# Performance work log

Measured on AMD Instinct MI355X. Metric: run time of the kernel, lower is better.

The kernel has to match this reference:

```python
import jax, jax.numpy as jnp
import numpy as np

K = 3
STRIDE = 1
PAD = 1


def _unfold(x, k, stride, pad):
    # x: (B, C, H, W) -> (B, C*k*k, L) matching torch.nn.functional.unfold
    # ordering: channel slowest, then kh, then kw.
    B, C, H, W = x.shape
    Hout = (H + 2 * pad - k) // stride + 1
    Wout = (W + 2 * pad - k) // stride + 1
    xp = jnp.pad(x, ((0, 0), (0, 0), (pad, pad), (pad, pad)))
    patches = []  # fixed k*k loop (9 iters), not a data-dim loop
    for i in range(k):
        for j in range(k):
            patches.append(xp[:, :, i:i + stride * Hout:stride, j:j + stride * Wout:stride])
    # (B, C, k*k, Hout, Wout) -> (B, C*k*k, L)
    p = jnp.stack(patches, axis=2)
    return p.reshape(B, C * k * k, Hout * Wout), Hout, Wout


def setup_inputs() -> dict:
    key = jax.random.key(0)
    k1, k2 = jax.random.split(key)
    x = jax.random.normal(k1, (4, 32, 56, 56), dtype=jnp.float32)
    weights = jax.random.normal(k2, (64, 32, 3, 3), dtype=jnp.float32)
    return {"x": x, "weights": weights}


def reference(x, weights):
    B = x.shape[0]
    O = weights.shape[0]
    mu_w = jnp.mean(jnp.abs(weights))
    x_unf, Hout, Wout = _unfold(x, K, STRIDE, PAD)      # (B, Ckk, L)
    w_unf = weights.reshape(O, -1)                        # (O, Ckk)
    # min-plus 'convolution': broadcast min then reduce over patch dim
    min_val = jnp.minimum(x_unf[:, None, :, :], w_unf[None, :, :, None])  # (B, O, Ckk, L)
    z = mu_w * jnp.sum(min_val, axis=2)                   # (B, O, L)
    return z.reshape(B, O, Hout, Wout)
```

## Files before the change

kernel.cpp:

```cpp
#include <hip/hip_runtime.h>

#define CIN  32
#define OCH  64
#define HH   56
#define WW   56
#define BB   4
#define OT   4
#define IMG  (HH * WW)
#define NW   18432
#define PH   58
#define PW   58
#define PIMG (PH * PW)
#define NXPK (BB * (CIN/2) * PIMG)
#define XPKBLKS (NXPK / 256)
#define NWPK (OCH * (CIN/2) * 9)
#define WPKBLKS (NWPK / 256)
#define WOFFu 64
#define XOFFu (WOFFu + NWPK)

typedef _Float16 h2 __attribute__((ext_vector_type(2)));

static __device__ __forceinline__ h2 pkmin_vs(h2 xv, unsigned wu) {
    unsigned xu = __builtin_bit_cast(unsigned, xv);
    unsigned ru;
    asm("v_pk_min_f16 %0, %1, %2" : "=v"(ru) : "v"(xu), "s"(wu));
    return __builtin_bit_cast(h2, ru);
}

__global__ __launch_bounds__(256) void prep(const float* __restrict__ x,
                                            const float* __restrict__ w,
                                            float* __restrict__ ws) {
    unsigned* wsu = reinterpret_cast<unsigned*>(ws);
    if (blockIdx.x < XPKBLKS) {
        int idx = blockIdx.x * 256 + threadIdx.x;
        int bc  = idx / PIMG;
        int r   = idx - bc * PIMG;
        int ph  = r / PW;
        int pw  = r - ph * PW;
        int hh  = ph - 1, wc = pw - 1;
        float v0 = 0.f, v1 = 0.f;
        if ((unsigned)hh < (unsigned)HH && (unsigned)wc < (unsigned)WW) {
            int base = ((bc >> 4) * CIN + (bc & 15) * 2) * IMG + hh * WW + wc;
            v0 = x[base];
            v1 = x[base + IMG];
        }
        h2 p; p.x = (_Float16)v0; p.y = (_Float16)v1;
        wsu[XOFFu + idx] = __builtin_bit_cast(unsigned, p);
        return;
    }
    if (blockIdx.x < XPKBLKS + WPKBLKS) {
        int idx = (blockIdx.x - XPKBLKS) * 256 + threadIdx.x;
        int t    = idx % 9;
        int rest = idx / 9;
        int cp   = rest & 15;
        int oo   = rest >> 4;
        int base = oo * (CIN * 9) + cp * 18 + t;
        h2 p; p.x = (_Float16)w[base]; p.y = (_Float16)w[base + 9];
        wsu[WOFFu + idx] = __builtin_bit_cast(unsigned, p);
        return;
    }
    float s = 0.f;
    const float4* w4 = reinterpret_cast<const float4*>(w);
    #pragma unroll
    for (int k = 0; k < 18; ++k) {
        float4 v = w4[k * 256 + threadIdx.x];
        s += fabsf(v.x) + fabsf(v.y) + fabsf(v.z) + fabsf(v.w);
    }
    #pragma unroll
    for (int off = 32; off; off >>= 1) s += __shfl_down(s, off);
    __shared__ float sm[4];
    if ((threadIdx.x & 63) == 0) sm[threadIdx.x >> 6] = s;
    __syncthreads();
    if (threadIdx.x == 0)
        ws[0] = (sm[0] + sm[1] + sm[2] + sm[3]) * (1.0f / (float)NW);
}

__global__ __launch_bounds__(128) void minconv_kernel(const float* __restrict__ ws,
                                                      const float* __restrict__ wts,
                                                      float* __restrict__ out) {
    const unsigned* wsu = reinterpret_cast<const unsigned*>(ws);
    const int lane = threadIdx.x & 63;
    const int wv   = threadIdx.x >> 6;
    const int wvs  = __builtin_amdgcn_readfirstlane(wv);
    const int hw = blockIdx.x * 64 + lane;
    const int o0 = blockIdx.y * OT;
    const int b  = blockIdx.z;
    const int h  = hw / WW;
    const int w  = hw - h * WW;

    const float mu = ws[0];

    const int cp0 = wvs * 8;
    const unsigned* xq = wsu + XOFFu + (size_t)(b * 16 + cp0) * PIMG + h * PW + w;
    const unsigned* wq0 = wsu + WOFFu + o0 * 144 + cp0 * 9;

    h2 xall[72];
    #pragma unroll
    for (int cp = 0; cp < 8; ++cp)
        #pragma unroll
        for (int kh = 0; kh < 3; ++kh)
            #pragma unroll
            for (int kw = 0; kw < 3; ++kw)
                xall[cp * 9 + kh * 3 + kw] =
                    __builtin_bit_cast(h2, xq[cp * PIMG + kh * PW + kw]);

    h2 ones; ones.x = (_Float16)1.f; ones.y = (_Float16)1.f;
    float acc0 = 0.f, acc1 = 0.f, acc2 = 0.f, acc3 = 0.f;

    unsigned wA[36], wB[36];
    #pragma unroll
    for (int i = 0; i < 36; ++i) wA[i] = wq0[i];

    #pragma unroll
    for (int oo = 0; oo < OT; ++oo) {
        #pragma unroll
        for (int i = 0; i < 36; ++i) wB[i] = wq0[oo * 144 + 36 + i];

        float ae = 0.f, ao = 0.f;
        #pragma unroll
        for (int cp = 0; cp < 4; ++cp)
            #pragma unroll
            for (int t = 0; t < 9; ++t) {
                h2 m = pkmin_vs(xall[cp * 9 + t], wA[cp * 9 + t]);
                if (t & 1) ao = __builtin_amdgcn_fdot2(m, ones, ao, false);
                else       ae = __builtin_amdgcn_fdot2(m, ones, ae, false);
            }

        if (oo < OT - 1) {
            #pragma unroll
            for (int i = 0; i < 36; ++i) wA[i] = wq0[(oo + 1) * 144 + i];
        }

        #pragma unroll
        for (int cp = 0; cp < 4; ++cp)
            #pragma unroll
            for (int t = 0; t < 9; ++t) {
                h2 m = pkmin_vs(xall[(cp + 4) * 9 + t], wB[cp * 9 + t]);
                if (t & 1) ao = __builtin_amdgcn_fdot2(m, ones, ao, false);
                else       ae = __builtin_amdgcn_fdot2(m, ones, ae, false);
            }

        float a = ae + ao;
        switch (oo) {
            case 0: acc0 = a; break;
            case 1: acc1 = a; break;
            case 2: acc2 = a; break;
            case 3: acc3 = a; break;
        }
    }

    __shared__ float red[2][2][64];
    if (wv == 0) {
        red[0][0][lane] = acc2;
        red[0][1][lane] = acc3;
    } else {
        red[1][0][lane] = acc0;
        red[1][1][lane] = acc1;
    }
    __syncthreads();

    float* ob = out + ((size_t)b * OCH + o0) * IMG + hw;
    if (wv == 0) {
        ob[0]       = mu * (acc0 + red[1][0][lane]);
        ob[IMG]     = mu * (acc1 + red[1][1][lane]);
    } else {
        ob[2 * IMG] = mu * (acc2 + red[0][0][lane]);
        ob[3 * IMG] = mu * (acc3 + red[0][1][lane]);
    }
}

extern "C" void kernel_launch(void* const* d_in, const int* in_sizes, int n_in,
                              void* d_out, int out_size, void* d_ws, size_t ws_size,
                              hipStream_t stream) {
    const float* x   = (const float*)d_in[0];
    const float* w   = (const float*)d_in[1];
    float*       out = (float*)d_out;
    float*       ws  = (float*)d_ws;

    prep<<<XPKBLKS + WPKBLKS + 1, 256, 0, stream>>>(x, w, ws);
    dim3 grid(IMG / 64, OCH / OT, BB);
    minconv_kernel<<<grid, 128, 0, stream>>>(ws, w, out);
}
```

Measured before the change: 68.60 us.

## Sum min-products with packed fp16 adds and re-layout weights contiguously per wave

The per-element fdot2 accumulations are replaced by a tree of v_pk_add_f16 over each channel pair's nine taps. A single fdot2 then folds each partial sum into the fp32 accumulator. This cuts the reduction instruction count and shortens the dependency chain. The weight packing is reordered so each wave's weights for an output tile are contiguous, which should make the scalar weight loads simpler. The cost is that nine-term sums are now accumulated in fp16, which reduces precision.

```diff
diff --git a/kernel.cpp b/kernel.cpp
--- a/kernel.cpp
+++ b/kernel.cpp
@@ -26,6 +26,13 @@
     asm("v_pk_min_f16 %0, %1, %2" : "=v"(ru) : "v"(xu), "s"(wu));
     return __builtin_bit_cast(h2, ru);
 }
+static __device__ __forceinline__ h2 pkadd(h2 a, h2 b) {
+    unsigned au = __builtin_bit_cast(unsigned, a);
+    unsigned bu = __builtin_bit_cast(unsigned, b);
+    unsigned ru;
+    asm("v_pk_add_f16 %0, %1, %2" : "=v"(ru) : "v"(au), "v"(bu));
+    return __builtin_bit_cast(h2, ru);
+}
 
 __global__ __launch_bounds__(256) void prep(const float* __restrict__ x,
                                             const float* __restrict__ w,
@@ -50,12 +57,18 @@
     }
     if (blockIdx.x < XPKBLKS + WPKBLKS) {
         int idx = (blockIdx.x - XPKBLKS) * 256 + threadIdx.x;
-        int t    = idx % 9;
-        int rest = idx / 9;
-        int cp   = rest & 15;
-        int oo   = rest >> 4;
-        int base = oo * (CIN * 9) + cp * 18 + t;
-        h2 p; p.x = (_Float16)w[base]; p.y = (_Float16)w[base + 9];
+        int otile = idx / 576;
+        int r     = idx - otile * 576;
+        int wvq   = r / 288;
+        int r2    = r - wvq * 288;
+        int oo    = r2 / 72;
+        int r3    = r2 - oo * 72;
+        int cl    = r3 / 9;
+        int t     = r3 - cl * 9;
+        int o     = otile * OT + oo;
+        int cp    = wvq * 8 + cl;
+        int src   = o * (CIN * 9) + cp * 18 + t;
+        h2 p; p.x = (_Float16)w[src]; p.y = (_Float16)w[src + 9];
         wsu[WOFFu + idx] = __builtin_bit_cast(unsigned, p);
         return;
     }
@@ -92,7 +105,7 @@
 
     const int cp0 = wvs * 8;
     const unsigned* xq = wsu + XOFFu + (size_t)(b * 16 + cp0) * PIMG + h * PW + w;
-    const unsigned* wq0 = wsu + WOFFu + o0 * 144 + cp0 * 9;
+    const unsigned* wq0 = wsu + WOFFu + blockIdx.y * 576 + wvs * 288;
 
     h2 xall[72];
     #pragma unroll
@@ -114,33 +127,40 @@
     #pragma unroll
     for (int oo = 0; oo < OT; ++oo) {
         #pragma unroll
-        for (int i = 0; i < 36; ++i) wB[i] = wq0[oo * 144 + 36 + i];
-
-        float ae = 0.f, ao = 0.f;
-        #pragma unroll
-        for (int cp = 0; cp < 4; ++cp)
-            #pragma unroll
-            for (int t = 0; t < 9; ++t) {
-                h2 m = pkmin_vs(xall[cp * 9 + t], wA[cp * 9 + t]);
-                if (t & 1) ao = __builtin_amdgcn_fdot2(m, ones, ao, false);
-                else       ae = __builtin_amdgcn_fdot2(m, ones, ae, false);
-            }
+        for (int i = 0; i < 36; ++i) wB[i] = wq0[oo * 72 + 36 + i];
+
+        float a = 0.f;
+        #pragma unroll
+        for (int cl = 0; cl < 4; ++cl) {
+            h2 m[9];
+            #pragma unroll
+            for (int t = 0; t < 9; ++t)
+                m[t] = pkmin_vs(xall[cl * 9 + t], wA[cl * 9 + t]);
+            h2 t01 = pkadd(m[0], m[1]), t23 = pkadd(m[2], m[3]);
+            h2 t45 = pkadd(m[4], m[5]), t67 = pkadd(m[6], m[7]);
+            h2 q0 = pkadd(t01, t23), q1 = pkadd(t45, t67);
+            h2 s9 = pkadd(pkadd(q0, q1), m[8]);
+            a = __builtin_amdgcn_fdot2(s9, ones, a, false);
+        }
 
         if (oo < OT - 1) {
             #pragma unroll
-            for (int i = 0; i < 36; ++i) wA[i] = wq0[(oo + 1) * 144 + i];
-        }
-
-        #pragma unroll
-        for (int cp = 0; cp < 4; ++cp)
-            #pragma unroll
-            for (int t = 0; t < 9; ++t) {
-                h2 m = pkmin_vs(xall[(cp + 4) * 9 + t], wB[cp * 9 + t]);
-                if (t & 1) ao = __builtin_amdgcn_fdot2(m, ones, ao, false);
-                else       ae = __builtin_amdgcn_fdot2(m, ones, ae, false);
-            }
-
-        float a = ae + ao;
+            for (int i = 0; i < 36; ++i) wA[i] = wq0[(oo + 1) * 72 + i];
+        }
+
+        #pragma unroll
+        for (int cl = 0; cl < 4; ++cl) {
+            h2 m[9];
+            #pragma unroll
+            for (int t = 0; t < 9; ++t)
+                m[t] = pkmin_vs(xall[(cl + 4) * 9 + t], wB[cl * 9 + t]);
+            h2 t01 = pkadd(m[0], m[1]), t23 = pkadd(m[2], m[3]);
+            h2 t45 = pkadd(m[4], m[5]), t67 = pkadd(m[6], m[7]);
+            h2 q0 = pkadd(t01, t23), q1 = pkadd(t45, t67);
+            h2 s9 = pkadd(pkadd(q0, q1), m[8]);
+            a = __builtin_amdgcn_fdot2(s9, ones, a, false);
+        }
+
         switch (oo) {
             case 0: acc0 = a; break;
             case 1: acc1 = a; break;
```

Result: no change. 68.27 us (-0.5%).
